# Kernel optimization log

Hardware: AMD Instinct MI355X
Metric: run time of the kernel (lower is better)

Reference implementation:

```python
import jax, jax.numpy as jnp
import numpy as np

HIDDEN_DIM = 128
NEIGHBOR_K = 2
N_ROWS = 1_000_000
BATCH = 262_144


def setup_inputs() -> dict:
    key = jax.random.key(0)
    k1, k2, k3, k4 = jax.random.split(key, 4)
    D = HIDDEN_DIM
    cat = D * (2 * NEIGHBOR_K + 1)  # 640
    x_rows = jax.random.normal(k1, (N_ROWS, D), dtype=jnp.float32)
    seed_indices = jax.random.randint(k2, (BATCH,), 0, N_ROWS)
    # torch.nn.Linear params: W [out, in], b [out]
    W1 = jax.random.normal(k3, (D, cat), dtype=jnp.float32) * (1.0 / np.sqrt(cat))
    b1 = jnp.zeros((D,), dtype=jnp.float32)
    W2 = jax.random.normal(k4, (D, D), dtype=jnp.float32) * (1.0 / np.sqrt(D))
    b2 = jnp.zeros((D,), dtype=jnp.float32)
    return {"x_rows": x_rows, "seed_indices": seed_indices,
            "W1": W1, "b1": b1, "W2": W2, "b2": b2}


def reference(x_rows, seed_indices, W1, b1, W2, b2):
    N, D = x_rows.shape
    B = seed_indices.shape[0]
    offsets = jnp.arange(-NEIGHBOR_K, NEIGHBOR_K + 1)  # [2k+1]
    idx = jnp.clip(seed_indices[:, None] + offsets[None, :], 0, N - 1)  # [B, 2k+1]
    # gather neighbor rows and flatten -> same as torch.cat(chunks, dim=-1)
    x_cat = x_rows[idx].reshape(B, (2 * NEIGHBOR_K + 1) * D)  # [B, 5D]
    h = jax.nn.relu(x_cat @ W1.T + b1)  # [B, D]
    return h @ W2.T + b2  # [B, D]
```

## Files before the change

kernel.cpp:

```cpp
#include <hip/hip_runtime.h>
#include <hip/hip_bf16.h>

#define D 128
#define CAT 640
#define BM 32
#define W1F_ELEMS 81920
#define W2F_ELEMS 16384

typedef __attribute__((ext_vector_type(8))) short bf16x8;
typedef __attribute__((ext_vector_type(4))) float f32x4;

static __device__ __forceinline__ unsigned short f32_to_bf16(float f) {
    unsigned u = __float_as_uint(f);
    unsigned r = u + 0x7FFFu + ((u >> 16) & 1u);
    return (unsigned short)(r >> 16);
}

static __device__ __forceinline__ unsigned pack_bf16x2(float a, float b) {
    __hip_bfloat162 h = __float22bfloat162_rn(make_float2(a, b));
    return *reinterpret_cast<unsigned*>(&h);
}

static __device__ __forceinline__ void gload_lds16(const float* g, void* lds) {
    __builtin_amdgcn_global_load_lds(
        (const __attribute__((address_space(1))) void*)g,
        (__attribute__((address_space(3))) void*)lds, 16, 0, 0);
}

__global__ void prep_frags(const float* __restrict__ W1, const float* __restrict__ W2,
                           unsigned short* __restrict__ W1f, unsigned short* __restrict__ W2f) {
    int f = blockIdx.x * 256 + threadIdx.x;
    if (f < W1F_ELEMS) {
        int e = f & 7, l = (f >> 3) & 63, j16 = (f >> 9) & 7, ks = f >> 12;
        int o = j16 * 16 + (l & 15);
        int k = ks * 32 + ((l >> 4) << 3) + e;
        W1f[f] = f32_to_bf16(W1[o * CAT + k]);
    } else if (f < W1F_ELEMS + W2F_ELEMS) {
        int f2 = f - W1F_ELEMS;
        int e = f2 & 7, l = (f2 >> 3) & 63, j16 = (f2 >> 9) & 7, ks = f2 >> 12;
        int o = j16 * 16 + (l & 15);
        int k = ks * 32 + ((l >> 4) << 3) + e;
        W2f[f2] = f32_to_bf16(W2[o * D + k]);
    }
}

__global__ __launch_bounds__(256, 4) void rowmlp_kernel(
    const float* __restrict__ x_rows, const int* __restrict__ seeds,
    const unsigned short* __restrict__ W1f, const float* __restrict__ b1,
    const unsigned short* __restrict__ W2f, const float* __restrict__ b2,
    float* __restrict__ out, int Nrows)
{
    __shared__ __align__(16) unsigned char smem[2][16384];
    __shared__ int sseed[BM];

    const int tid = threadIdx.x;
    const int blk = blockIdx.x;

    if (tid < BM) sseed[tid] = seeds[blk * BM + tid];
    __syncthreads();

    const int w   = tid >> 6;
    const int l   = tid & 63;
    const int l15 = l & 15;
    const int lhi = l >> 4;

    int sbase[4], scoff[4];
    #pragma unroll
    for (int i = 0; i < 4; ++i) {
        int r = 8 * w + 2 * i + (l >> 5);
        sbase[i] = sseed[r];
        scoff[i] = ((l & 31) ^ (r & 7)) << 2;
    }

#define ISSUE(J)                                                               \
    {                                                                          \
        _Pragma("unroll")                                                      \
        for (int i = 0; i < 4; ++i) {                                          \
            int idx = sbase[i] + (J) - 2;                                      \
            idx = idx < 0 ? 0 : (idx >= Nrows ? Nrows - 1 : idx);              \
            gload_lds16(x_rows + (size_t)idx * D + scoff[i],                   \
                        (void*)(smem[(J) & 1] + w * 4096 + i * 1024));         \
        }                                                                      \
    }

    ISSUE(0)

    const bf16x8* W1v = (const bf16x8*)W1f;
    const bf16x8* W2v = (const bf16x8*)W2f;

    f32x4 acc[2][2] = {};

    #pragma unroll
    for (int j = 0; j < 5; ++j) {
        asm volatile("s_waitcnt vmcnt(0)" ::: "memory");
        __builtin_amdgcn_s_barrier();
        if (j < 4) ISSUE(j + 1)

        const float* buf = (const float*)smem[j & 1];
        #pragma unroll
        for (int ks = 0; ks < 4; ++ks) {
            bf16x8 a[2];
            #pragma unroll
            for (int m = 0; m < 2; ++m) {
                const int r = m * 16 + l15;
                const int s = r & 7;
                const int cc = ks * 8 + lhi * 2;
                float4 q0 = *(const float4*)(buf + r * 128 + (((cc) ^ s) << 2));
                float4 q1 = *(const float4*)(buf + r * 128 + (((cc + 1) ^ s) << 2));
                union { unsigned u[4]; bf16x8 v; } pk;
                pk.u[0] = pack_bf16x2(q0.x, q0.y);
                pk.u[1] = pack_bf16x2(q0.z, q0.w);
                pk.u[2] = pack_bf16x2(q1.x, q1.y);
                pk.u[3] = pack_bf16x2(q1.z, q1.w);
                a[m] = pk.v;
            }
            #pragma unroll
            for (int n = 0; n < 2; ++n) {
                const int j16 = w * 2 + n;
                bf16x8 b = W1v[((j * 4 + ks) * 8 + j16) * 64 + l];
                #pragma unroll
                for (int m = 0; m < 2; ++m)
                    acc[m][n] = __builtin_amdgcn_mfma_f32_16x16x32_bf16(a[m], b, acc[m][n], 0, 0, 0);
            }
        }
    }
#undef ISSUE

    unsigned short (*Hb)[D] = (unsigned short (*)[D])smem[1];
    #pragma unroll
    for (int n = 0; n < 2; ++n) {
        const int col = w * 32 + n * 16 + l15;
        const float bias = b1[col];
        #pragma unroll
        for (int m = 0; m < 2; ++m) {
            #pragma unroll
            for (int r = 0; r < 4; ++r) {
                float v = acc[m][n][r] + bias;
                v = v > 0.f ? v : 0.f;
                const int row = m * 16 + lhi * 4 + r;
                Hb[row][col ^ ((row & 7) << 3)] = f32_to_bf16(v);
            }
        }
    }
    __syncthreads();

    f32x4 acc2[2][2] = {};
    #pragma unroll
    for (int ks = 0; ks < 4; ++ks) {
        bf16x8 a2[2], bb[2];
        #pragma unroll
        for (int m = 0; m < 2; ++m) {
            const int row = m * 16 + l15;
            a2[m] = *(const bf16x8*)(&Hb[row][(ks * 32 + lhi * 8) ^ ((row & 7) << 3)]);
        }
        #pragma unroll
        for (int n = 0; n < 2; ++n) {
            const int j16 = w * 2 + n;
            bb[n] = W2v[(ks * 8 + j16) * 64 + l];
        }
        #pragma unroll
        for (int m = 0; m < 2; ++m)
            #pragma unroll
            for (int n = 0; n < 2; ++n)
                acc2[m][n] = __builtin_amdgcn_mfma_f32_16x16x32_bf16(a2[m], bb[n], acc2[m][n], 0, 0, 0);
    }

    #pragma unroll
    for (int n = 0; n < 2; ++n) {
        const int col = w * 32 + n * 16 + l15;
        const float bias = b2[col];
        #pragma unroll
        for (int m = 0; m < 2; ++m) {
            #pragma unroll
            for (int r = 0; r < 4; ++r) {
                const int row = m * 16 + lhi * 4 + r;
                out[(size_t)(blk * BM + row) * D + col] = acc2[m][n][r] + bias;
            }
        }
    }
}

extern "C" void kernel_launch(void* const* d_in, const int* in_sizes, int n_in,
                              void* d_out, int out_size, void* d_ws, size_t ws_size,
                              hipStream_t stream) {
    const float* x_rows = (const float*)d_in[0];
    const int*   seeds  = (const int*)d_in[1];
    const float* W1     = (const float*)d_in[2];
    const float* b1     = (const float*)d_in[3];
    const float* W2     = (const float*)d_in[4];
    const float* b2     = (const float*)d_in[5];
    float* out = (float*)d_out;

    int Nrows = in_sizes[0] / D;
    int B = in_sizes[1];

    unsigned short* W1f = (unsigned short*)d_ws;
    unsigned short* W2f = W1f + W1F_ELEMS;

    prep_frags<<<(W1F_ELEMS + W2F_ELEMS + 255) / 256, 256, 0, stream>>>(W1, W2, W1f, W2f);
    rowmlp_kernel<<<B / BM, 256, 0, stream>>>(x_rows, seeds, W1f, b1, W2f, b2, out, Nrows);
}
```

Before: 192.6 us.

## Make row-MLP blocks persistent over 8 tiles with triple-buffered gather pipeline

New measurement: 370.0 us. 1.92x slower.

```diff
diff --git a/kernel.cpp b/kernel.cpp
--- a/kernel.cpp
+++ b/kernel.cpp
@@ -4,6 +4,7 @@
 #define D 128
 #define CAT 640
 #define BM 32
+#define NG 8
 #define W1F_ELEMS 81920
 #define W2F_ELEMS 16384
 
@@ -44,140 +45,165 @@
     }
 }
 
-__global__ __launch_bounds__(256, 4) void rowmlp_kernel(
+__global__ __launch_bounds__(256, 3) void rowmlp_kernel(
     const float* __restrict__ x_rows, const int* __restrict__ seeds,
     const unsigned short* __restrict__ W1f, const float* __restrict__ b1,
     const unsigned short* __restrict__ W2f, const float* __restrict__ b2,
     float* __restrict__ out, int Nrows)
 {
-    __shared__ __align__(16) unsigned char smem[2][16384];
-    __shared__ int sseed[BM];
+    __shared__ __align__(16) unsigned char Ab[3][16384];
+    __shared__ __align__(16) unsigned short Hb[16][D];
+    __shared__ int sseed[2][BM];
 
     const int tid = threadIdx.x;
     const int blk = blockIdx.x;
-
-    if (tid < BM) sseed[tid] = seeds[blk * BM + tid];
-    __syncthreads();
-
     const int w   = tid >> 6;
     const int l   = tid & 63;
     const int l15 = l & 15;
     const int lhi = l >> 4;
 
-    int sbase[4], scoff[4];
+    int srow[4], scoff[4], sbase[4];
     #pragma unroll
     for (int i = 0; i < 4; ++i) {
-        int r = 8 * w + 2 * i + (l >> 5);
-        sbase[i] = sseed[r];
-        scoff[i] = ((l & 31) ^ (r & 7)) << 2;
-    }
-
-#define ISSUE(J)                                                               \
+        srow[i]  = 8 * w + 2 * i + (l >> 5);
+        scoff[i] = ((l & 31) ^ (srow[i] & 7)) << 2;
+    }
+
+    if (tid < BM) sseed[0][tid] = seeds[(blk * NG) * BM + tid];
+    __syncthreads();
+    #pragma unroll
+    for (int i = 0; i < 4; ++i) sbase[i] = sseed[0][srow[i]];
+
+    const bf16x8* W1v = (const bf16x8*)W1f;
+    const bf16x8* W2v = (const bf16x8*)W2f;
+
+#define WAIT4 asm volatile("s_waitcnt vmcnt(4)" ::: "memory")
+#define WAIT0 asm volatile("s_waitcnt vmcnt(0)" ::: "memory")
+#define BAR   __builtin_amdgcn_s_barrier()
+
+#define ISSUE(NB, DST)                                                         \
     {                                                                          \
         _Pragma("unroll")                                                      \
         for (int i = 0; i < 4; ++i) {                                          \
-            int idx = sbase[i] + (J) - 2;                                      \
+            int idx = sbase[i] + (NB) - 2;                                     \
             idx = idx < 0 ? 0 : (idx >= Nrows ? Nrows - 1 : idx);              \
             gload_lds16(x_rows + (size_t)idx * D + scoff[i],                   \
-                        (void*)(smem[(J) & 1] + w * 4096 + i * 1024));         \
+                        (void*)((DST) + w * 4096 + i * 1024));                 \
         }                                                                      \
     }
 
-    ISSUE(0)
-
-    const bf16x8* W1v = (const bf16x8*)W1f;
-    const bf16x8* W2v = (const bf16x8*)W2f;
-
-    f32x4 acc[2][2] = {};
-
-    #pragma unroll
-    for (int j = 0; j < 5; ++j) {
-        asm volatile("s_waitcnt vmcnt(0)" ::: "memory");
-        __builtin_amdgcn_s_barrier();
-        if (j < 4) ISSUE(j + 1)
-
-        const float* buf = (const float*)smem[j & 1];
+#define COMPUTE(SRC, NB)                                                       \
+    {                                                                          \
+        const float* buf = (const float*)(SRC);                                \
+        _Pragma("unroll")                                                      \
+        for (int ks = 0; ks < 4; ++ks) {                                       \
+            bf16x8 a[2];                                                       \
+            _Pragma("unroll")                                                  \
+            for (int m = 0; m < 2; ++m) {                                      \
+                const int r = m * 16 + l15;                                    \
+                const int s = r & 7;                                           \
+                const int cc = ks * 8 + lhi * 2;                               \
+                float4 q0 = *(const float4*)(buf + r * 128 + (((cc) ^ s) << 2));     \
+                float4 q1 = *(const float4*)(buf + r * 128 + (((cc + 1) ^ s) << 2)); \
+                union { unsigned u[4]; bf16x8 v; } pk;                         \
+                pk.u[0] = pack_bf16x2(q0.x, q0.y);                             \
+                pk.u[1] = pack_bf16x2(q0.z, q0.w);                             \
+                pk.u[2] = pack_bf16x2(q1.x, q1.y);                             \
+                pk.u[3] = pack_bf16x2(q1.z, q1.w);                             \
+                a[m] = pk.v;                                                   \
+            }                                                                  \
+            _Pragma("unroll")                                                  \
+            for (int n = 0; n < 2; ++n) {                                      \
+                bf16x8 b = W1v[(((NB) * 4 + ks) * 8 + (w * 2 + n)) * 64 + l];  \
+                _Pragma("unroll")                                              \
+                for (int m = 0; m < 2; ++m)                                    \
+                    acc[m][n] = __builtin_amdgcn_mfma_f32_16x16x32_bf16(a[m], b, acc[m][n], 0, 0, 0); \
+            }                                                                  \
+        }                                                                      \
+    }
+
+    unsigned char* c0 = Ab[0];
+    unsigned char* c1 = Ab[1];
+    unsigned char* c2 = Ab[2];
+#define ROT { unsigned char* t = c0; c0 = c1; c1 = c2; c2 = t; }
+
+    ISSUE(0, c0)
+    ISSUE(1, c1)
+
+    for (int g = 0; g < NG; ++g) {
+        f32x4 acc[2][2] = {};
+
+        WAIT4; BAR;
+        if (g < NG - 1 && tid < BM)
+            sseed[(g + 1) & 1][tid] = seeds[(blk * NG + g + 1) * BM + tid];
+        ISSUE(2, c2)
+        COMPUTE(c0, 0)
+        ROT
+        WAIT4; BAR;
+        ISSUE(3, c2)
+        COMPUTE(c0, 1)
+        ROT
+        WAIT4; BAR;
+        ISSUE(4, c2)
+        COMPUTE(c0, 2)
+        ROT
+        WAIT4; BAR;
+        if (g < NG - 1) {
+            #pragma unroll
+            for (int i = 0; i < 4; ++i) sbase[i] = sseed[(g + 1) & 1][srow[i]];
+            ISSUE(0, c2)
+        }
+        COMPUTE(c0, 3)
+        ROT
+        if (g < NG - 1) { WAIT4; } else { WAIT0; }
+        BAR;
+        if (g < NG - 1) ISSUE(1, c2)
+        COMPUTE(c0, 4)
+        ROT
+
+        const size_t obase = (size_t)(blk * NG + g) * BM;
         #pragma unroll
-        for (int ks = 0; ks < 4; ++ks) {
-            bf16x8 a[2];
-            #pragma unroll
-            for (int m = 0; m < 2; ++m) {
-                const int r = m * 16 + l15;
-                const int s = r & 7;
-                const int cc = ks * 8 + lhi * 2;
-                float4 q0 = *(const float4*)(buf + r * 128 + (((cc) ^ s) << 2));
-                float4 q1 = *(const float4*)(buf + r * 128 + (((cc + 1) ^ s) << 2));
-                union { unsigned u[4]; bf16x8 v; } pk;
-                pk.u[0] = pack_bf16x2(q0.x, q0.y);
-                pk.u[1] = pack_bf16x2(q0.z, q0.w);
-                pk.u[2] = pack_bf16x2(q1.x, q1.y);
-                pk.u[3] = pack_bf16x2(q1.z, q1.w);
-                a[m] = pk.v;
+        for (int ph = 0; ph < 2; ++ph) {
+            #pragma unroll
+            for (int n = 0; n < 2; ++n) {
+                const int col = w * 32 + n * 16 + l15;
+                const float bias = b1[col];
+                #pragma unroll
+                for (int r = 0; r < 4; ++r) {
+                    const int row = lhi * 4 + r;
+                    float v = acc[ph][n][r] + bias;
+                    v = v > 0.f ? v : 0.f;
+                    Hb[row][col ^ ((row & 7) << 3)] = f32_to_bf16(v);
+                }
             }
+            __syncthreads();
+            f32x4 acc2[2] = {};
+            #pragma unroll
+            for (int ks = 0; ks < 4; ++ks) {
+                bf16x8 a2 = *(const bf16x8*)(&Hb[l15][(ks * 32 + lhi * 8) ^ ((l15 & 7) << 3)]);
+                #pragma unroll
+                for (int n = 0; n < 2; ++n) {
+                    bf16x8 bb = W2v[(ks * 8 + w * 2 + n) * 64 + l];
+                    acc2[n] = __builtin_amdgcn_mfma_f32_16x16x32_bf16(a2, bb, acc2[n], 0, 0, 0);
+                }
+            }
             #pragma unroll
             for (int n = 0; n < 2; ++n) {
-                const int j16 = w * 2 + n;
-                bf16x8 b = W1v[((j * 4 + ks) * 8 + j16) * 64 + l];
+                const int col = w * 32 + n * 16 + l15;
+                const float bias = b2[col];
                 #pragma unroll
-                for (int m = 0; m < 2; ++m)
-                    acc[m][n] = __builtin_amdgcn_mfma_f32_16x16x32_bf16(a[m], b, acc[m][n], 0, 0, 0);
+                for (int r = 0; r < 4; ++r)
+                    out[(obase + ph * 16 + lhi * 4 + r) * D + col] = acc2[n][r] + bias;
             }
+            if (ph == 0) __syncthreads();
         }
     }
 #undef ISSUE
-
-    unsigned short (*Hb)[D] = (unsigned short (*)[D])smem[1];
-    #pragma unroll
-    for (int n = 0; n < 2; ++n) {
-        const int col = w * 32 + n * 16 + l15;
-        const float bias = b1[col];
-        #pragma unroll
-        for (int m = 0; m < 2; ++m) {
-            #pragma unroll
-            for (int r = 0; r < 4; ++r) {
-                float v = acc[m][n][r] + bias;
-                v = v > 0.f ? v : 0.f;
-                const int row = m * 16 + lhi * 4 + r;
-                Hb[row][col ^ ((row & 7) << 3)] = f32_to_bf16(v);
-            }
-        }
-    }
-    __syncthreads();
-
-    f32x4 acc2[2][2] = {};
-    #pragma unroll
-    for (int ks = 0; ks < 4; ++ks) {
-        bf16x8 a2[2], bb[2];
-        #pragma unroll
-        for (int m = 0; m < 2; ++m) {
-            const int row = m * 16 + l15;
-            a2[m] = *(const bf16x8*)(&Hb[row][(ks * 32 + lhi * 8) ^ ((row & 7) << 3)]);
-        }
-        #pragma unroll
-        for (int n = 0; n < 2; ++n) {
-            const int j16 = w * 2 + n;
-            bb[n] = W2v[(ks * 8 + j16) * 64 + l];
-        }
-        #pragma unroll
-        for (int m = 0; m < 2; ++m)
-            #pragma unroll
-            for (int n = 0; n < 2; ++n)
-                acc2[m][n] = __builtin_amdgcn_mfma_f32_16x16x32_bf16(a2[m], bb[n], acc2[m][n], 0, 0, 0);
-    }
-
-    #pragma unroll
-    for (int n = 0; n < 2; ++n) {
-        const int col = w * 32 + n * 16 + l15;
-        const float bias = b2[col];
-        #pragma unroll
-        for (int m = 0; m < 2; ++m) {
-            #pragma unroll
-            for (int r = 0; r < 4; ++r) {
-                const int row = m * 16 + lhi * 4 + r;
-                out[(size_t)(blk * BM + row) * D + col] = acc2[m][n][r] + bias;
-            }
-        }
-    }
+#undef COMPUTE
+#undef ROT
+#undef WAIT4
+#undef WAIT0
+#undef BAR
 }
 
 extern "C" void kernel_launch(void* const* d_in, const int* in_sizes, int n_in,
@@ -198,5 +224,6 @@
     unsigned short* W2f = W1f + W1F_ELEMS;
 
     prep_frags<<<(W1F_ELEMS + W2F_ELEMS + 255) / 256, 256, 0, stream>>>(W1, W2, W1f, W2f);
-    rowmlp_kernel<<<B / BM, 256, 0, stream>>>(x_rows, seeds, W1f, b1, W2f, b2, out, Nrows);
-}
+    int nblocks = B / (NG * BM);
+    rowmlp_kernel<<<nblocks, 256, 0, stream>>>(x_rows, seeds, W1f, b1, W2f, b2, out, Nrows);
+}
```

## Bucket-sort seeds so each block streams a contiguous row span once

Applied to the files above, without the earlier changes.

After: 248.0 us. 28.8% more time.

```diff
diff --git a/kernel.cpp b/kernel.cpp
--- a/kernel.cpp
+++ b/kernel.cpp
@@ -2,8 +2,8 @@
 #include <hip/hip_bf16.h>
 
 #define D 128
-#define CAT 640
-#define BM 32
+#define SPANMAX 192
+#define NBUCK 65536
 #define W1F_ELEMS 81920
 #define W2F_ELEMS 16384
 
@@ -19,12 +19,6 @@
 static __device__ __forceinline__ unsigned pack_bf16x2(float a, float b) {
     __hip_bfloat162 h = __float22bfloat162_rn(make_float2(a, b));
     return *reinterpret_cast<unsigned*>(&h);
-}
-
-static __device__ __forceinline__ void gload_lds16(const float* g, void* lds) {
-    __builtin_amdgcn_global_load_lds(
-        (const __attribute__((address_space(1))) void*)g,
-        (__attribute__((address_space(3))) void*)lds, 16, 0, 0);
 }
 
 __global__ void prep_frags(const float* __restrict__ W1, const float* __restrict__ W2,
@@ -34,7 +28,7 @@
         int e = f & 7, l = (f >> 3) & 63, j16 = (f >> 9) & 7, ks = f >> 12;
         int o = j16 * 16 + (l & 15);
         int k = ks * 32 + ((l >> 4) << 3) + e;
-        W1f[f] = f32_to_bf16(W1[o * CAT + k]);
+        W1f[f] = f32_to_bf16(W1[o * 640 + k]);
     } else if (f < W1F_ELEMS + W2F_ELEMS) {
         int f2 = f - W1F_ELEMS;
         int e = f2 & 7, l = (f2 >> 3) & 63, j16 = (f2 >> 9) & 7, ks = f2 >> 12;
@@ -44,89 +38,154 @@
     }
 }
 
-__global__ __launch_bounds__(256, 4) void rowmlp_kernel(
-    const float* __restrict__ x_rows, const int* __restrict__ seeds,
+__global__ void zero_counts(int* __restrict__ counts) {
+    counts[blockIdx.x * 256 + threadIdx.x] = 0;
+}
+
+__global__ void hist_kernel(const int* __restrict__ seeds, int* __restrict__ counts, int B) {
+    int i = blockIdx.x * 256 + threadIdx.x;
+    if (i < B) atomicAdd(&counts[seeds[i] >> 4], 1);
+}
+
+__global__ __launch_bounds__(1024) void scan_kernel(const int* __restrict__ counts,
+                                                    int* __restrict__ offsets) {
+    __shared__ int tsum[1024];
+    const int tid = threadIdx.x;
+    const int base = tid * 64;
+    int s = 0;
+    for (int i = 0; i < 64; ++i) s += counts[base + i];
+    tsum[tid] = s;
+    __syncthreads();
+    for (int off = 1; off < 1024; off <<= 1) {
+        int v = 0;
+        if (tid >= off) v = tsum[tid - off];
+        __syncthreads();
+        if (tid >= off) tsum[tid] += v;
+        __syncthreads();
+    }
+    int run = tsum[tid] - s;
+    for (int i = 0; i < 64; ++i) { offsets[base + i] = run; run += counts[base + i]; }
+}
+
+__global__ void scatter_kernel(const int* __restrict__ seeds, int* __restrict__ offsets,
+                               int2* __restrict__ sorted, int B) {
+    int i = blockIdx.x * 256 + threadIdx.x;
+    if (i < B) {
+        int s = seeds[i];
+        int pos = atomicAdd(&offsets[s >> 4], 1);
+        sorted[pos] = make_int2(s, i);
+    }
+}
+
+__global__ __launch_bounds__(256, 3) void rowmlp_kernel(
+    const float* __restrict__ x_rows, const int2* __restrict__ sorted,
     const unsigned short* __restrict__ W1f, const float* __restrict__ b1,
     const unsigned short* __restrict__ W2f, const float* __restrict__ b2,
     float* __restrict__ out, int Nrows)
 {
-    __shared__ __align__(16) unsigned char smem[2][16384];
-    __shared__ int sseed[BM];
+    __shared__ __align__(16) unsigned short tile[SPANMAX * 128];
+    __shared__ int sseed[32], sorg[32], sctl[2];
 
     const int tid = threadIdx.x;
-    const int blk = blockIdx.x;
-
-    if (tid < BM) sseed[tid] = seeds[blk * BM + tid];
-    __syncthreads();
+    const int blk = (blockIdx.x & 7) * 1024 + (blockIdx.x >> 3);
+
+    if (tid < 64) {
+        int2 p = sorted[blk * 32 + (tid & 31)];
+        if (tid < 32) { sseed[tid] = p.x; sorg[tid] = p.y; }
+        int mn = p.x, mx = p.x;
+        #pragma unroll
+        for (int k = 32; k >= 1; k >>= 1) {
+            mn = min(mn, __shfl_xor(mn, k));
+            mx = max(mx, __shfl_xor(mx, k));
+        }
+        if (tid == 0) {
+            int lo = mn - 2; lo = lo < 0 ? 0 : lo;
+            int hi = mx + 2; hi = hi > Nrows - 1 ? Nrows - 1 : hi;
+            sctl[0] = lo; sctl[1] = hi - lo + 1;
+        }
+    }
+    __syncthreads();
+
+    const int lo = sctl[0], span = sctl[1];
+    const bool stream = (span <= SPANMAX);
 
     const int w   = tid >> 6;
     const int l   = tid & 63;
     const int l15 = l & 15;
     const int lhi = l >> 4;
 
-    int sbase[4], scoff[4];
-    #pragma unroll
-    for (int i = 0; i < 4; ++i) {
-        int r = 8 * w + 2 * i + (l >> 5);
-        sbase[i] = sseed[r];
-        scoff[i] = ((l & 31) ^ (r & 7)) << 2;
-    }
-
-#define ISSUE(J)                                                               \
-    {                                                                          \
-        _Pragma("unroll")                                                      \
-        for (int i = 0; i < 4; ++i) {                                          \
-            int idx = sbase[i] + (J) - 2;                                      \
-            idx = idx < 0 ? 0 : (idx >= Nrows ? Nrows - 1 : idx);              \
-            gload_lds16(x_rows + (size_t)idx * D + scoff[i],                   \
-                        (void*)(smem[(J) & 1] + w * 4096 + i * 1024));         \
-        }                                                                      \
-    }
-
-    ISSUE(0)
+    int rA0[5], rA1[5];
+    {
+        const int s0 = sseed[l15], s1 = sseed[16 + l15];
+        #pragma unroll
+        for (int j = 0; j < 5; ++j) {
+            if (stream) {
+                int i0 = s0 + j - 2; i0 = i0 < 0 ? 0 : (i0 > Nrows - 1 ? Nrows - 1 : i0);
+                int i1 = s1 + j - 2; i1 = i1 < 0 ? 0 : (i1 > Nrows - 1 ? Nrows - 1 : i1);
+                rA0[j] = i0 - lo; rA1[j] = i1 - lo;
+            } else {
+                rA0[j] = l15 * 5 + j; rA1[j] = (16 + l15) * 5 + j;
+            }
+        }
+    }
+
+    if (stream) {
+        const int total = span * 16;
+        #pragma unroll
+        for (int it = 0; it < 12; ++it) {
+            int q = tid + it * 256;
+            if (q < total) {
+                int row = q >> 4, c = q & 15;
+                const float4* src = (const float4*)(x_rows + (size_t)(lo + row) * D + c * 8);
+                float4 v0 = src[0], v1 = src[1];
+                union { unsigned u[4]; bf16x8 v; } pk;
+                pk.u[0] = pack_bf16x2(v0.x, v0.y); pk.u[1] = pack_bf16x2(v0.z, v0.w);
+                pk.u[2] = pack_bf16x2(v1.x, v1.y); pk.u[3] = pack_bf16x2(v1.z, v1.w);
+                *(bf16x8*)(&tile[row * 128 + ((c ^ (row & 7)) * 8)]) = pk.v;
+            }
+        }
+    } else {
+        #pragma unroll
+        for (int it = 0; it < 10; ++it) {
+            int q = tid + it * 256;
+            int rw = q >> 4, c = q & 15;
+            int sidx = (rw * 205) >> 10;
+            int j = rw - sidx * 5;
+            int sr = sseed[sidx] + j - 2;
+            sr = sr < 0 ? 0 : (sr > Nrows - 1 ? Nrows - 1 : sr);
+            const float4* src = (const float4*)(x_rows + (size_t)sr * D + c * 8);
+            float4 v0 = src[0], v1 = src[1];
+            union { unsigned u[4]; bf16x8 v; } pk;
+            pk.u[0] = pack_bf16x2(v0.x, v0.y); pk.u[1] = pack_bf16x2(v0.z, v0.w);
+            pk.u[2] = pack_bf16x2(v1.x, v1.y); pk.u[3] = pack_bf16x2(v1.z, v1.w);
+            *(bf16x8*)(&tile[rw * 128 + ((c ^ (rw & 7)) * 8)]) = pk.v;
+        }
+    }
+    __syncthreads();
 
     const bf16x8* W1v = (const bf16x8*)W1f;
     const bf16x8* W2v = (const bf16x8*)W2f;
 
     f32x4 acc[2][2] = {};
-
     #pragma unroll
     for (int j = 0; j < 5; ++j) {
-        asm volatile("s_waitcnt vmcnt(0)" ::: "memory");
-        __builtin_amdgcn_s_barrier();
-        if (j < 4) ISSUE(j + 1)
-
-        const float* buf = (const float*)smem[j & 1];
+        const int r0 = rA0[j], r1 = rA1[j];
         #pragma unroll
         for (int ks = 0; ks < 4; ++ks) {
-            bf16x8 a[2];
-            #pragma unroll
-            for (int m = 0; m < 2; ++m) {
-                const int r = m * 16 + l15;
-                const int s = r & 7;
-                const int cc = ks * 8 + lhi * 2;
-                float4 q0 = *(const float4*)(buf + r * 128 + (((cc) ^ s) << 2));
-                float4 q1 = *(const float4*)(buf + r * 128 + (((cc + 1) ^ s) << 2));
-                union { unsigned u[4]; bf16x8 v; } pk;
-                pk.u[0] = pack_bf16x2(q0.x, q0.y);
-                pk.u[1] = pack_bf16x2(q0.z, q0.w);
-                pk.u[2] = pack_bf16x2(q1.x, q1.y);
-                pk.u[3] = pack_bf16x2(q1.z, q1.w);
-                a[m] = pk.v;
-            }
+            const int ch = ks * 4 + lhi;
+            bf16x8 a0 = *(const bf16x8*)(&tile[r0 * 128 + ((ch ^ (r0 & 7)) * 8)]);
+            bf16x8 a1 = *(const bf16x8*)(&tile[r1 * 128 + ((ch ^ (r1 & 7)) * 8)]);
             #pragma unroll
             for (int n = 0; n < 2; ++n) {
-                const int j16 = w * 2 + n;
-                bf16x8 b = W1v[((j * 4 + ks) * 8 + j16) * 64 + l];
-                #pragma unroll
-                for (int m = 0; m < 2; ++m)
-                    acc[m][n] = __builtin_amdgcn_mfma_f32_16x16x32_bf16(a[m], b, acc[m][n], 0, 0, 0);
-            }
-        }
-    }
-#undef ISSUE
-
-    unsigned short (*Hb)[D] = (unsigned short (*)[D])smem[1];
+                bf16x8 b = W1v[((j * 4 + ks) * 8 + (w * 2 + n)) * 64 + l];
+                acc[0][n] = __builtin_amdgcn_mfma_f32_16x16x32_bf16(a0, b, acc[0][n], 0, 0, 0);
+                acc[1][n] = __builtin_amdgcn_mfma_f32_16x16x32_bf16(a1, b, acc[1][n], 0, 0, 0);
+            }
+        }
+    }
+    __syncthreads();
+
+    unsigned short (*Hb)[128] = (unsigned short (*)[128])tile;
     #pragma unroll
     for (int n = 0; n < 2; ++n) {
         const int col = w * 32 + n * 16 + l15;
@@ -144,7 +203,11 @@
     }
     __syncthreads();
 
-    f32x4 acc2[2][2] = {};
+    #pragma unroll
+    for (int m = 0; m < 2; ++m)
+        #pragma unroll
+        for (int n = 0; n < 2; ++n)
+            acc[m][n] = (f32x4){0.f, 0.f, 0.f, 0.f};
     #pragma unroll
     for (int ks = 0; ks < 4; ++ks) {
         bf16x8 a2[2], bb[2];
@@ -154,15 +217,13 @@
             a2[m] = *(const bf16x8*)(&Hb[row][(ks * 32 + lhi * 8) ^ ((row & 7) << 3)]);
         }
         #pragma unroll
-        for (int n = 0; n < 2; ++n) {
-            const int j16 = w * 2 + n;
-            bb[n] = W2v[(ks * 8 + j16) * 64 + l];
-        }
+        for (int n = 0; n < 2; ++n)
+            bb[n] = W2v[(ks * 8 + (w * 2 + n)) * 64 + l];
         #pragma unroll
         for (int m = 0; m < 2; ++m)
             #pragma unroll
             for (int n = 0; n < 2; ++n)
-                acc2[m][n] = __builtin_amdgcn_mfma_f32_16x16x32_bf16(a2[m], bb[n], acc2[m][n], 0, 0, 0);
+                acc[m][n] = __builtin_amdgcn_mfma_f32_16x16x32_bf16(a2[m], bb[n], acc[m][n], 0, 0, 0);
     }
 
     #pragma unroll
@@ -174,7 +235,7 @@
             #pragma unroll
             for (int r = 0; r < 4; ++r) {
                 const int row = m * 16 + lhi * 4 + r;
-                out[(size_t)(blk * BM + row) * D + col] = acc2[m][n][r] + bias;
+                out[(size_t)sorg[row] * D + col] = acc[m][n][r] + bias;
             }
         }
     }
@@ -196,7 +257,14 @@
 
     unsigned short* W1f = (unsigned short*)d_ws;
     unsigned short* W2f = W1f + W1F_ELEMS;
+    int* counts  = (int*)(W2f + W2F_ELEMS);
+    int* offsets = counts + NBUCK;
+    int2* sorted = (int2*)(offsets + NBUCK);
 
     prep_frags<<<(W1F_ELEMS + W2F_ELEMS + 255) / 256, 256, 0, stream>>>(W1, W2, W1f, W2f);
-    rowmlp_kernel<<<B / BM, 256, 0, stream>>>(x_rows, seeds, W1f, b1, W2f, b2, out, Nrows);
-}
+    zero_counts<<<NBUCK / 256, 256, 0, stream>>>(counts);
+    hist_kernel<<<(B + 255) / 256, 256, 0, stream>>>(seeds, counts, B);
+    scan_kernel<<<1, 1024, 0, stream>>>(counts, offsets);
+    scatter_kernel<<<(B + 255) / 256, 256, 0, stream>>>(seeds, offsets, sorted, B);
+    rowmlp_kernel<<<B / 32, 256, 0, stream>>>(x_rows, sorted, W1f, b1, W2f, b2, out, Nrows);
+}
```
